# Optimization experiments

Hardware: AMD Instinct MI355X
Metric: run time of the kernel (lower is better)

Reference implementation:

```python
import jax, jax.numpy as jnp
import numpy as np

D_MODEL = 64
D_K = 64
D_V = 64
SEQ = 8192
MASK_VAL = 10.0 ** 10  # matches original: scores - 1e10 * triu_mask


def setup_inputs() -> dict:
    key = jax.random.key(0)
    ks = jax.random.split(key, 7)
    s = 1.0 / np.sqrt(D_MODEL)
    return {
        "x": jax.random.normal(ks[0], (SEQ, D_MODEL), dtype=jnp.float32),
        "w_q": jax.random.uniform(ks[1], (D_K, D_MODEL), jnp.float32, -s, s),
        "b_q": jax.random.uniform(ks[2], (D_K,), jnp.float32, -s, s),
        "w_k": jax.random.uniform(ks[3], (D_K, D_MODEL), jnp.float32, -s, s),
        "b_k": jax.random.uniform(ks[4], (D_K,), jnp.float32, -s, s),
        "w_v": jax.random.uniform(ks[5], (D_V, D_MODEL), jnp.float32, -s, s),
        "b_v": jax.random.uniform(ks[6], (D_V,), jnp.float32, -s, s),
    }


def reference(x, w_q, b_q, w_k, b_k, w_v, b_v):
    # torch Linear: y = x @ W.T + b
    q = x @ w_q.T + b_q            # [S, d_k]
    k = x @ w_k.T + b_k            # [S, d_k]
    v = x @ w_v.T + b_v            # [S, d_v]
    scores = (q @ k.T) / jnp.sqrt(jnp.float32(D_K))  # [S, S]
    S = scores.shape[0]
    # upper-triangular (strict) causal mask, subtracted with large constant
    mask = jnp.triu(jnp.ones((S, S), dtype=scores.dtype), k=1)
    attn = jax.nn.softmax(scores - MASK_VAL * mask, axis=1)
    return attn @ v                # [S, d_v]
```

## Files before the change

### kernel.cpp

```cpp
#include <hip/hip_runtime.h>

#define SEQ 8192
#define DM 64

typedef __bf16 bfrag __attribute__((ext_vector_type(8)));
typedef __bf16 b4v   __attribute__((ext_vector_type(4)));
typedef float  f4    __attribute__((ext_vector_type(4)));

union PW { int w[4]; bfrag v; };

#define QSCALE 0.1803368801111204f

__device__ inline float fexp2(float x) {
    float y;
    asm("v_exp_f32 %0, %1" : "=v"(y) : "v"(x));
    return y;
}

__device__ inline int cvtpk(float a, float b) {
    int d;
    asm("v_cvt_pk_bf16_f32 %0, %1, %2" : "=v"(d) : "v"(a), "v"(b));
    return d;
}

__device__ inline void split8(const float* __restrict__ p, bfrag& hi, bfrag& lo) {
    #pragma unroll
    for (int e = 0; e < 8; ++e) {
        const float v = p[e];
        const __bf16 h = (__bf16)v;
        hi[e] = h;
        lo[e] = (__bf16)(v - (float)h);
    }
}

__global__ __launch_bounds__(256) void qkv_proj(
    const float* __restrict__ x,
    const float* __restrict__ wq, const float* __restrict__ bq,
    const float* __restrict__ wk, const float* __restrict__ bk,
    const float* __restrict__ wv, const float* __restrict__ bv,
    __bf16* __restrict__ Qb, __bf16* __restrict__ Ks, __bf16* __restrict__ Vg)
{
    const int lane = threadIdx.x & 63;
    const int wid  = threadIdx.x >> 6;
    const int task = blockIdx.x * 4 + wid;
    const int m    = task >> 11;
    const int rest = task & 2047;
    const int rt   = rest >> 2;
    const int dt   = rest & 3;
    const int rb   = rt << 4;
    const int g = lane >> 4, r = lane & 15;

    const float* w = (m == 0) ? wq : (m == 1) ? wk : wv;

    bfrag xhi[2], xlo[2];
    #pragma unroll
    for (int kh = 0; kh < 2; ++kh)
        split8(x + (rb + r) * DM + kh * 32 + g * 8, xhi[kh], xlo[kh]);
    bfrag whi[2], wlo[2];
    #pragma unroll
    for (int kh = 0; kh < 2; ++kh)
        split8(w + (dt * 16 + r) * DM + kh * 32 + g * 8, whi[kh], wlo[kh]);

    if (m < 2) {
        f4 acc = {0.f, 0.f, 0.f, 0.f};
        #pragma unroll
        for (int kh = 0; kh < 2; ++kh) {
            acc = __builtin_amdgcn_mfma_f32_16x16x32_bf16(whi[kh], xhi[kh], acc, 0, 0, 0);
            acc = __builtin_amdgcn_mfma_f32_16x16x32_bf16(wlo[kh], xhi[kh], acc, 0, 0, 0);
            acc = __builtin_amdgcn_mfma_f32_16x16x32_bf16(whi[kh], xlo[kh], acc, 0, 0, 0);
        }
        const float* bias = (m == 0) ? bq : bk;
        const int c0 = dt * 16 + g * 4;
        const float4 b4 = *(const float4*)(bias + c0);
        const float sc = (m == 0) ? QSCALE : 1.0f;
        b4v pv;
        pv[0] = (__bf16)((acc[0] + b4.x) * sc);
        pv[1] = (__bf16)((acc[1] + b4.y) * sc);
        pv[2] = (__bf16)((acc[2] + b4.z) * sc);
        pv[3] = (__bf16)((acc[3] + b4.w) * sc);
        if (m == 0) {
            *(b4v*)(Qb + (rb + r) * DM + c0) = pv;
        } else {
            const int row = rb + r, t = row >> 5, row32 = row & 31;
            const int ch  = dt * 2 + (g >> 1);
            const int b2  = ((row32 >> 4) << 1) | (ch >> 2);
            *(b4v*)(Ks + t * 2048 + b2 * 512 + (ch & 3) * 128
                       + (row32 & 15) * 8 + (g & 1) * 4) = pv;
        }
    } else {
        f4 acc = {0.f, 0.f, 0.f, 0.f};
        #pragma unroll
        for (int kh = 0; kh < 2; ++kh) {
            acc = __builtin_amdgcn_mfma_f32_16x16x32_bf16(xhi[kh], whi[kh], acc, 0, 0, 0);
            acc = __builtin_amdgcn_mfma_f32_16x16x32_bf16(xlo[kh], whi[kh], acc, 0, 0, 0);
            acc = __builtin_amdgcn_mfma_f32_16x16x32_bf16(xhi[kh], wlo[kh], acc, 0, 0, 0);
        }
        const int d  = dt * 16 + r;
        const float bd = bv[d];
        const int L0 = (rb & 31) + g * 4;
        const int P0 = ((L0 & 15) >> 2) * 8 + (L0 >> 4) * 4;
        const int t  = rb >> 5;
        b4v pv;
        pv[0] = (__bf16)(acc[0] + bd);
        pv[1] = (__bf16)(acc[1] + bd);
        pv[2] = (__bf16)(acc[2] + bd);
        pv[3] = (__bf16)(acc[3] + bd);
        *(b4v*)(Vg + t * 2048 + (d >> 4) * 512 + (P0 >> 3) * 128
                   + (d & 15) * 8 + (P0 & 7)) = pv;
    }
}

__global__ __launch_bounds__(256)
__attribute__((amdgpu_waves_per_eu(4)))
void flash_attn(
    const __bf16* __restrict__ Qb, const __bf16* __restrict__ Ks,
    const __bf16* __restrict__ Vg,
    float* __restrict__ Opart, float* __restrict__ Lpart)
{
    __shared__ __align__(16) unsigned char smem[34816];

    const int tid  = threadIdx.x;
    const int lane = tid & 63;
    const int wid  = tid >> 6;
    const int b    = blockIdx.x;
    const int fam  = b >> 2;
    const int g4   = b & 3;
    const int grp  = fam >> 6, hh = fam & 63;
    const int qt   = (grp == 0) ? (255 - hh) : (grp == 1) ? hh
                   : (grp == 2) ? (191 - hh) : (64 + hh);
    const int qbase = qt * 32;
    const int gq = lane >> 4;
    const int r  = lane & 15;
    const int lo16 = lane << 4;

    bfrag qf[2][2];
    #pragma unroll
    for (int sub = 0; sub < 2; ++sub)
        #pragma unroll
        for (int kh = 0; kh < 2; ++kh)
            qf[sub][kh] = *(const bfrag*)(Qb + (qbase + sub * 16 + r) * DM + kh * 32 + gq * 8);

    bfrag ones;
    #pragma unroll
    for (int e = 0; e < 8; ++e) ones[e] = (__bf16)1.0f;

    f4 o[2][4] = {};
    f4 lsacc[2] = {};

    const char* Kbb = (const char*)Ks;
    const char* Vbb = (const char*)Vg;

    const int jw = g4 * 4 + wid;
    const int nlive = (qt >= jw) ? ((qt - jw) >> 4) + 1 : 0;

    for (int s = 0; s < nlive; ++s) {
        const int j = jw + s * 16;
        const long long jb = (long long)j * 4096;
        const bfrag kf0 = *(const bfrag*)(Kbb + jb + lo16);
        const bfrag kf1 = *(const bfrag*)(Kbb + jb + 1024 + lo16);
        const bfrag kf2 = *(const bfrag*)(Kbb + jb + 2048 + lo16);
        const bfrag kf3 = *(const bfrag*)(Kbb + jb + 3072 + lo16);
        bfrag vf[4];
        #pragma unroll
        for (int dt = 0; dt < 4; ++dt)
            vf[dt] = *(const bfrag*)(Vbb + jb + dt * 1024 + lo16);

        const int kvb = j * 32 + gq * 4;
        #pragma unroll
        for (int sub = 0; sub < 2; ++sub) {
            f4 sh0 = {}, sh1 = {};
            sh0 = __builtin_amdgcn_mfma_f32_16x16x32_bf16(kf0, qf[sub][0], sh0, 0, 0, 0);
            sh0 = __builtin_amdgcn_mfma_f32_16x16x32_bf16(kf1, qf[sub][1], sh0, 0, 0, 0);
            sh1 = __builtin_amdgcn_mfma_f32_16x16x32_bf16(kf2, qf[sub][0], sh1, 0, 0, 0);
            sh1 = __builtin_amdgcn_mfma_f32_16x16x32_bf16(kf3, qf[sub][1], sh1, 0, 0, 0);

            float p0[4], p1[4];
            if (j < qt) {
                #pragma unroll
                for (int e = 0; e < 4; ++e) {
                    p0[e] = fexp2(sh0[e]);
                    p1[e] = fexp2(sh1[e]);
                }
            } else {
                const int qg = qbase + sub * 16 + r;
                #pragma unroll
                for (int e = 0; e < 4; ++e) {
                    p0[e] = (kvb + e      <= qg) ? fexp2(sh0[e]) : 0.f;
                    p1[e] = (kvb + e + 16 <= qg) ? fexp2(sh1[e]) : 0.f;
                }
            }

            PW pu;
            pu.w[0] = cvtpk(p0[0], p0[1]); pu.w[1] = cvtpk(p0[2], p0[3]);
            pu.w[2] = cvtpk(p1[0], p1[1]); pu.w[3] = cvtpk(p1[2], p1[3]);

            lsacc[sub] = __builtin_amdgcn_mfma_f32_16x16x32_bf16(pu.v, ones, lsacc[sub], 0, 0, 0);
            #pragma unroll
            for (int dt = 0; dt < 4; ++dt)
                o[sub][dt] = __builtin_amdgcn_mfma_f32_16x16x32_bf16(pu.v, vf[dt], o[sub][dt], 0, 0, 0);
        }
    }

    float* Ol  = (float*)smem;
    float* Lsm = (float*)(smem + 33792);
    #pragma unroll
    for (int sub = 0; sub < 2; ++sub) {
        if (r == 0)
            #pragma unroll
            for (int e = 0; e < 4; ++e)
                Lsm[wid * 32 + sub * 16 + gq * 4 + e] = lsacc[sub][e];
        #pragma unroll
        for (int dt = 0; dt < 4; ++dt)
            #pragma unroll
            for (int e = 0; e < 4; ++e)
                Ol[(wid * 32 + sub * 16 + gq * 4 + e) * 66 + dt * 16 + r] = o[sub][dt][e];
    }
    __syncthreads();

    for (int i = tid; i < 32 * 64; i += 256) {
        const int row = i >> 6, col = i & 63;
        const float sum = Ol[(row) * 66 + col] + Ol[(32 + row) * 66 + col]
                        + Ol[(64 + row) * 66 + col] + Ol[(96 + row) * 66 + col];
        Opart[((long long)g4 * SEQ + qbase + row) * DM + col] = sum;
    }
    if (tid < 32) {
        const float l = Lsm[tid] + Lsm[32 + tid] + Lsm[64 + tid] + Lsm[96 + tid];
        Lpart[g4 * SEQ + qbase + tid] = l;
    }
}

__global__ __launch_bounds__(256) void normalize(
    const float* __restrict__ Opart, const float* __restrict__ Lpart,
    float* __restrict__ out)
{
    const int i = blockIdx.x * 256 + threadIdx.x;
    const f4* O = (const f4*)Opart;
    const int N = SEQ * DM / 4;
    const int row = i >> 4;
    const f4 a0 = O[i], a1 = O[N + i], a2 = O[2 * N + i], a3 = O[3 * N + i];
    const float l = (Lpart[row] + Lpart[SEQ + row])
                  + (Lpart[2 * SEQ + row] + Lpart[3 * SEQ + row]);
    const float inv = 1.0f / l;
    f4 res;
    #pragma unroll
    for (int e = 0; e < 4; ++e) res[e] = ((a0[e] + a1[e]) + (a2[e] + a3[e])) * inv;
    ((f4*)out)[i] = res;
}

extern "C" void kernel_launch(void* const* d_in, const int* in_sizes, int n_in,
                              void* d_out, int out_size, void* d_ws, size_t ws_size,
                              hipStream_t stream)
{
    (void)in_sizes; (void)n_in; (void)out_size; (void)ws_size;
    const float* x  = (const float*)d_in[0];
    const float* wq = (const float*)d_in[1];
    const float* bq = (const float*)d_in[2];
    const float* wk = (const float*)d_in[3];
    const float* bk = (const float*)d_in[4];
    const float* wv = (const float*)d_in[5];
    const float* bv = (const float*)d_in[6];
    float* out = (float*)d_out;

    __bf16* Qb = (__bf16*)d_ws;
    __bf16* Ks = Qb + SEQ * DM;
    __bf16* Vg = Ks + SEQ * DM;
    float*  Opart = (float*)(Vg + SEQ * DM);
    float*  Lpart = Opart + 4 * SEQ * DM;

    qkv_proj<<<1536, 256, 0, stream>>>(x, wq, bq, wk, bk, wv, bv, Qb, Ks, Vg);
    flash_attn<<<1024, 256, 0, stream>>>(Qb, Ks, Vg, Opart, Lpart);
    normalize<<<SEQ * DM / 4 / 256, 256, 0, stream>>>(Opart, Lpart, out);
}
```

Baseline: 34.23 us.

## Process 64-query tiles per 512-thread block so warp pairs share K/V tiles

```diff
diff --git a/kernel.cpp b/kernel.cpp
--- a/kernel.cpp
+++ b/kernel.cpp
@@ -110,25 +110,26 @@
     }
 }
 
-__global__ __launch_bounds__(256)
+__global__ __launch_bounds__(512)
 __attribute__((amdgpu_waves_per_eu(4)))
 void flash_attn(
     const __bf16* __restrict__ Qb, const __bf16* __restrict__ Ks,
     const __bf16* __restrict__ Vg,
     float* __restrict__ Opart, float* __restrict__ Lpart)
 {
-    __shared__ __align__(16) unsigned char smem[34816];
+    __shared__ float Ol[4][32][66];
+    __shared__ float Lsm[8][32];
 
     const int tid  = threadIdx.x;
     const int lane = tid & 63;
     const int wid  = tid >> 6;
     const int b    = blockIdx.x;
     const int fam  = b >> 2;
-    const int g4   = b & 3;
-    const int grp  = fam >> 6, hh = fam & 63;
-    const int qt   = (grp == 0) ? (255 - hh) : (grp == 1) ? hh
-                   : (grp == 2) ? (191 - hh) : (64 + hh);
-    const int qbase = qt * 32;
+    const int slice = b & 3;
+    const int qt   = (fam < 64) ? (127 - fam) : (fam - 64);
+    const int qbase = qt * 64;
+    const int h    = wid & 1;
+    const int jj   = wid >> 1;
     const int gq = lane >> 4;
     const int r  = lane & 15;
     const int lo16 = lane << 4;
@@ -138,7 +139,7 @@
     for (int sub = 0; sub < 2; ++sub)
         #pragma unroll
         for (int kh = 0; kh < 2; ++kh)
-            qf[sub][kh] = *(const bfrag*)(Qb + (qbase + sub * 16 + r) * DM + kh * 32 + gq * 8);
+            qf[sub][kh] = *(const bfrag*)(Qb + (qbase + h * 32 + sub * 16 + r) * DM + kh * 32 + gq * 8);
 
     bfrag ones;
     #pragma unroll
@@ -150,11 +151,12 @@
     const char* Kbb = (const char*)Ks;
     const char* Vbb = (const char*)Vg;
 
-    const int jw = g4 * 4 + wid;
-    const int nlive = (qt >= jw) ? ((qt - jw) >> 4) + 1 : 0;
+    const int jmax = 2 * qt + h;
+    const int j0   = slice * 4 + jj;
+    const int nlive = (jmax >= j0) ? ((jmax - j0) >> 4) + 1 : 0;
 
     for (int s = 0; s < nlive; ++s) {
-        const int j = jw + s * 16;
+        const int j = j0 + (s << 4);
         const long long jb = (long long)j * 4096;
         const bfrag kf0 = *(const bfrag*)(Kbb + jb + lo16);
         const bfrag kf1 = *(const bfrag*)(Kbb + jb + 1024 + lo16);
@@ -175,14 +177,14 @@
             sh1 = __builtin_amdgcn_mfma_f32_16x16x32_bf16(kf3, qf[sub][1], sh1, 0, 0, 0);
 
             float p0[4], p1[4];
-            if (j < qt) {
+            if (j < jmax) {
                 #pragma unroll
                 for (int e = 0; e < 4; ++e) {
                     p0[e] = fexp2(sh0[e]);
                     p1[e] = fexp2(sh1[e]);
                 }
             } else {
-                const int qg = qbase + sub * 16 + r;
+                const int qg = qbase + h * 32 + sub * 16 + r;
                 #pragma unroll
                 for (int e = 0; e < 4; ++e) {
                     p0[e] = (kvb + e      <= qg) ? fexp2(sh0[e]) : 0.f;
@@ -201,31 +203,36 @@
         }
     }
 
-    float* Ol  = (float*)smem;
-    float* Lsm = (float*)(smem + 33792);
-    #pragma unroll
-    for (int sub = 0; sub < 2; ++sub) {
-        if (r == 0)
+    if (r == 0)
+        #pragma unroll
+        for (int sub = 0; sub < 2; ++sub)
             #pragma unroll
             for (int e = 0; e < 4; ++e)
-                Lsm[wid * 32 + sub * 16 + gq * 4 + e] = lsacc[sub][e];
-        #pragma unroll
-        for (int dt = 0; dt < 4; ++dt)
+                Lsm[wid][sub * 16 + gq * 4 + e] = lsacc[sub][e];
+
+    #pragma unroll
+    for (int ph = 0; ph < 2; ++ph) {
+        if (h == ph) {
             #pragma unroll
-            for (int e = 0; e < 4; ++e)
-                Ol[(wid * 32 + sub * 16 + gq * 4 + e) * 66 + dt * 16 + r] = o[sub][dt][e];
-    }
-    __syncthreads();
-
-    for (int i = tid; i < 32 * 64; i += 256) {
-        const int row = i >> 6, col = i & 63;
-        const float sum = Ol[(row) * 66 + col] + Ol[(32 + row) * 66 + col]
-                        + Ol[(64 + row) * 66 + col] + Ol[(96 + row) * 66 + col];
-        Opart[((long long)g4 * SEQ + qbase + row) * DM + col] = sum;
-    }
-    if (tid < 32) {
-        const float l = Lsm[tid] + Lsm[32 + tid] + Lsm[64 + tid] + Lsm[96 + tid];
-        Lpart[g4 * SEQ + qbase + tid] = l;
+            for (int sub = 0; sub < 2; ++sub)
+                #pragma unroll
+                for (int dt = 0; dt < 4; ++dt)
+                    #pragma unroll
+                    for (int e = 0; e < 4; ++e)
+                        Ol[jj][sub * 16 + gq * 4 + e][dt * 16 + r] = o[sub][dt][e];
+        }
+        __syncthreads();
+        for (int i = tid; i < 32 * 64; i += 512) {
+            const int row = i >> 6, col = i & 63;
+            const float sum = (Ol[0][row][col] + Ol[1][row][col])
+                            + (Ol[2][row][col] + Ol[3][row][col]);
+            Opart[((long long)slice * SEQ + qbase + ph * 32 + row) * DM + col] = sum;
+        }
+        if (tid < 32)
+            Lpart[slice * SEQ + qbase + ph * 32 + tid]
+                = (Lsm[ph][tid] + Lsm[ph + 2][tid])
+                + (Lsm[ph + 4][tid] + Lsm[ph + 6][tid]);
+        __syncthreads();
     }
 }
 
@@ -268,6 +275,6 @@
     float*  Lpart = Opart + 4 * SEQ * DM;
 
     qkv_proj<<<1536, 256, 0, stream>>>(x, wq, bq, wk, bk, wv, bv, Qb, Ks, Vg);
-    flash_attn<<<1024, 256, 0, stream>>>(Qb, Ks, Vg, Opart, Lpart);
+    flash_attn<<<512, 512, 0, stream>>>(Qb, Ks, Vg, Opart, Lpart);
     normalize<<<SEQ * DM / 4 / 256, 256, 0, stream>>>(Opart, Lpart, out);
 }
```

New measurement: 35.02 us. 2.3% more time.
